# Performance work log

Measured on AMD Instinct MI355X. Metric: run time of the kernel, lower is better.

## Reference

```python
import jax, jax.numpy as jnp
import numpy as np

COMMITMENT_COST = 0.25
N_EMBED = 1024
EMB_DIM = 256

def setup_inputs() -> dict:
    key = jax.random.key(0)
    k1, k2 = jax.random.split(key)
    z = jax.random.normal(k1, (32, EMB_DIM, 32, 32), dtype=jnp.float32)
    # embedding.weight.data.uniform_(-1/n_embed, 1/n_embed)
    embedding = jax.random.uniform(k2, (N_EMBED, EMB_DIM), dtype=jnp.float32,
                                   minval=-1.0 / N_EMBED, maxval=1.0 / N_EMBED)
    return {"z": z, "embedding": embedding}

def reference(z, embedding):
    # NCHW -> NHWC
    zp = jnp.transpose(z, (0, 2, 3, 1))            # [B,H,W,D]
    in_shape = zp.shape
    flat = zp.reshape(-1, in_shape[-1])            # [N,D]
    # squared L2 distances (argmin equivalent to p=2 cdist argmin)
    d2 = (jnp.sum(flat * flat, axis=1, keepdims=True)
          - 2.0 * (flat @ embedding.T)
          + jnp.sum(embedding * embedding, axis=1))  # [N,K]
    idx = jnp.argmin(d2, axis=1)                   # [N]
    # one-hot @ codebook == direct gather
    z_quant = embedding[idx].reshape(in_shape)     # [B,H,W,D]
    codebook_loss = jnp.mean((z_quant - jax.lax.stop_gradient(zp)) ** 2)
    commitment_loss = jnp.mean((zp - jax.lax.stop_gradient(z_quant)) ** 2)
    loss = codebook_loss + COMMITMENT_COST * commitment_loss
    # straight-through estimator
    z_st = zp + jax.lax.stop_gradient(z_quant - zp)
    z_st = jnp.transpose(z_st, (0, 3, 1, 2))       # NHWC -> NCHW
    return (z_st, loss, codebook_loss, commitment_loss)
```

## Files before the change

kernel.cpp:

```cpp
#include <hip/hip_runtime.h>
#include <hip/hip_bf16.h>
#include <stdint.h>


typedef short v8s __attribute__((ext_vector_type(8)));
typedef float v4f __attribute__((ext_vector_type(4)));

__device__ inline unsigned short f2bf(float f) {
    uint32_t u = __float_as_uint(f);
    return (unsigned short)((u + 0x7fffu + ((u >> 16) & 1u)) >> 16);
}

__global__ __launch_bounds__(512) void k_prep_a(const float* __restrict__ z,
                                                unsigned short* __restrict__ Abf) {
    int tid = threadIdx.x;
    int b = blockIdx.x >> 4, hw0 = (blockIdx.x & 15) << 6;
    int t15 = tid & 15, dblk = tid >> 4;
    const float* zp = z + ((size_t)b << 18) + (size_t)(dblk << 3) * 1024 + hw0 + (t15 << 2);
    float4 L[8];
#pragma unroll
    for (int j = 0; j < 8; j++)
        L[j] = *(const float4*)(zp + (size_t)j * 1024);
    const float* Lf = (const float*)L;
    v8s* Aout = (v8s*)Abf + ((size_t)(b * 1024 + hw0 + (t15 << 2))) * 32 + dblk;
#pragma unroll
    for (int c = 0; c < 4; c++) {
        union { v8s v; unsigned short s[8]; } u;
#pragma unroll
        for (int j = 0; j < 8; j++) u.s[j] = f2bf(Lf[j * 4 + c]);
        Aout[(size_t)c * 32] = u.v;
    }
}

__global__ __launch_bounds__(256) void k_prep_e(const float* __restrict__ E,
                                                unsigned short* __restrict__ Ebf,
                                                float* __restrict__ nE,
                                                float* __restrict__ accum) {
    int k = blockIdx.x, tid = threadIdx.x;
    float v = E[(size_t)k * 256 + tid];
    Ebf[(size_t)k * 256 + tid] = f2bf(v);
    float s = v * v;
#pragma unroll
    for (int off = 1; off < 64; off <<= 1) s += __shfl_xor(s, off);
    __shared__ float w4[4];
    if ((tid & 63) == 0) w4[tid >> 6] = s;
    __syncthreads();
    if (tid == 0) {
        nE[k] = 0.5f * (w4[0] + w4[1] + w4[2] + w4[3]);
        if (k == 0) accum[0] = 0.f;
    }
}

__global__ __launch_bounds__(512, 4) void k_argmin(
        const unsigned short* __restrict__ Abf,
        const unsigned short* __restrict__ Ebf,
        const float* __restrict__ nE,
        unsigned long long* __restrict__ cand) {
    __shared__ v8s B[4096];
    int tid = threadIdx.x;
    int lane = tid & 63, w = tid >> 6;
    int g = lane >> 4, m = lane & 15;
    int split = blockIdx.x & 7;
    int R0 = (blockIdx.x >> 3) << 8;
    int C0 = split << 7;

    const v8s* Ep = (const v8s*)Ebf;
#pragma unroll
    for (int k = 0; k < 8; k++) {
        int u = tid + (k << 9);
        int um = u & 15, ug = (u >> 4) & 3, udc = (u >> 6) & 7, uct = u >> 9;
        B[u] = Ep[(size_t)(C0 + uct * 16 + um) * 32 + udc * 4 + ug];
    }
    float ne[8];
#pragma unroll
    for (int ct = 0; ct < 8; ct++) ne[ct] = nE[C0 + ct * 16 + m];

    v8s a[2][8];
    const v8s* Ap = (const v8s*)Abf;
    int rbase = R0 + w * 32;
#pragma unroll
    for (int s = 0; s < 2; s++) {
        int row = rbase + s * 16 + m;
#pragma unroll
        for (int dc = 0; dc < 8; dc++)
            a[s][dc] = Ap[(size_t)row * 32 + dc * 4 + g];
    }
    __syncthreads();

    float best[2][4]; int bidx[2][4];
#pragma unroll
    for (int s = 0; s < 2; s++)
#pragma unroll
        for (int r = 0; r < 4; r++) { best[s][r] = 3.4e38f; bidx[s][r] = 0; }

#pragma unroll 1
    for (int ct = 0; ct < 8; ct++) {
        v4f acc0 = {0.f, 0.f, 0.f, 0.f}, acc1 = {0.f, 0.f, 0.f, 0.f};
#pragma unroll
        for (int dc = 0; dc < 8; dc++) {
            v8s bf = B[ct * 512 + dc * 64 + g * 16 + m];
            acc0 = __builtin_amdgcn_mfma_f32_16x16x32_bf16(a[0][dc], bf, acc0, 0, 0, 0);
            acc1 = __builtin_amdgcn_mfma_f32_16x16x32_bf16(a[1][dc], bf, acc1, 0, 0, 0);
        }
        int code = C0 + (ct << 4) + m;
        float nv = ne[ct];
#pragma unroll
        for (int r = 0; r < 4; r++) {
            float s0 = nv - acc0[r];
            if (s0 < best[0][r]) { best[0][r] = s0; bidx[0][r] = code; }
            float s1 = nv - acc1[r];
            if (s1 < best[1][r]) { best[1][r] = s1; bidx[1][r] = code; }
        }
    }

#pragma unroll
    for (int s = 0; s < 2; s++)
#pragma unroll
        for (int r = 0; r < 4; r++) {
            uint32_t sb = __float_as_uint(best[s][r]);
            sb = (sb & 0x80000000u) ? ~sb : (sb | 0x80000000u);
            unsigned long long pk = ((unsigned long long)sb << 32) | (uint32_t)bidx[s][r];
#pragma unroll
            for (int off = 1; off < 16; off <<= 1) {
                unsigned long long o = __shfl_xor(pk, off);
                if (o < pk) pk = o;
            }
            if (m == 0)
                cand[(size_t)split * 32768 + R0 + w * 32 + s * 16 + g * 4 + r] = pk;
        }
}

__global__ __launch_bounds__(256) void k_out(const float* __restrict__ z,
                                             const float* __restrict__ E,
                                             const unsigned long long* __restrict__ cand,
                                             float* __restrict__ out,
                                             float* __restrict__ accum) {
    __shared__ float et[256][33];
    __shared__ int   kk[32];
    __shared__ float w4[4];
    int bid = blockIdx.x;
    int b = bid >> 5, hw0 = (bid & 31) << 5;
    int tid = threadIdx.x;
    if (tid < 32) {
        int n = b * 1024 + hw0 + tid;
        unsigned long long bv = cand[n];
#pragma unroll
        for (int s = 1; s < 8; s++) {
            unsigned long long v = cand[(size_t)s * 32768 + n];
            if (v < bv) bv = v;
        }
        kk[tid] = (int)(bv & 0xffffffffu);
    }
    __syncthreads();
    for (int r = 0; r < 32; r++)
        et[tid][r] = E[(size_t)kk[r] * 256 + tid];
    __syncthreads();

    int c4 = (tid & 7) << 2, dt = tid >> 3;
    const float* zb = z + ((size_t)b << 18);
    float* ob = out + ((size_t)b << 18);
    float lsum = 0.f;
#pragma unroll
    for (int i = 0; i < 8; i++) {
        int d = dt + (i << 5);
        size_t o = (size_t)d * 1024 + hw0 + c4;
        const float4 zv = *(const float4*)(zb + o);
        float4 ev;
        ev.x = et[d][c4]; ev.y = et[d][c4 + 1]; ev.z = et[d][c4 + 2]; ev.w = et[d][c4 + 3];
        *(float4*)(ob + o) = ev;
        float dx = ev.x - zv.x, dy = ev.y - zv.y, dz2 = ev.z - zv.z, dw = ev.w - zv.w;
        lsum += dx * dx + dy * dy + dz2 * dz2 + dw * dw;
    }
#pragma unroll
    for (int off = 1; off < 64; off <<= 1) lsum += __shfl_xor(lsum, off);
    if ((tid & 63) == 0) w4[tid >> 6] = lsum;
    __syncthreads();
    if (tid == 0) atomicAdd(accum, w4[0] + w4[1] + w4[2] + w4[3]);
}

__global__ void k_loss(const float* __restrict__ accum, float* __restrict__ out) {
    if (threadIdx.x == 0) {
        float s = accum[0] * (1.0f / 8388608.0f);
        out[8388608] = 1.25f * s;
        out[8388609] = s;
        out[8388610] = s;
    }
}

extern "C" void kernel_launch(void* const* d_in, const int* in_sizes, int n_in,
                              void* d_out, int out_size, void* d_ws, size_t ws_size,
                              hipStream_t stream) {
    const float* z = (const float*)d_in[0];
    const float* E = (const float*)d_in[1];
    char* ws = (char*)d_ws;
    unsigned short*     Abf   = (unsigned short*)(ws);
    unsigned short*     Ebf   = (unsigned short*)(ws + 16777216);
    float*              nE    = (float*)(ws + 17301504);
    unsigned long long* cand  = (unsigned long long*)(ws + 17305600);
    float*              accum = (float*)(ws + 19402752);
    float* out = (float*)d_out;

    hipLaunchKernelGGL(k_prep_a, dim3(512),  dim3(512), 0, stream, z, Abf);
    hipLaunchKernelGGL(k_prep_e, dim3(1024), dim3(256), 0, stream, E, Ebf, nE, accum);
    hipLaunchKernelGGL(k_argmin, dim3(1024), dim3(512), 0, stream, Abf, Ebf, nE, cand);
    hipLaunchKernelGGL(k_out,    dim3(1024), dim3(256), 0, stream, z, E, cand, out, accum);
    hipLaunchKernelGGL(k_loss,   dim3(1),    dim3(64),  0, stream, accum, out);
}
```

Measured before the change: 141.1 us.

## Fuse argmin and output gather into one kernel with double-buffered codebook staging

Merges the distance/argmin kernel and the gather/loss kernel into one. Each block now owns 64 rows across all 1024 codes, so the 8-way code split, the candidate buffer and the cross-split reduction are gone. Codebook tiles are streamed into LDS through double-buffered global_load_lds while the MFMAs run. The cost is that every block rereads the whole bf16 codebook, and the grid drops to 512 blocks of 256 threads, which may leave the GPU less occupied.

```diff
diff --git a/kernel.cpp b/kernel.cpp
--- a/kernel.cpp
+++ b/kernel.cpp
@@ -51,131 +51,138 @@
     }
 }
 
-__global__ __launch_bounds__(512, 4) void k_argmin(
+__global__ __launch_bounds__(256, 2) void k_main(
         const unsigned short* __restrict__ Abf,
         const unsigned short* __restrict__ Ebf,
         const float* __restrict__ nE,
-        unsigned long long* __restrict__ cand) {
-    __shared__ v8s B[4096];
+        const float* __restrict__ z,
+        const float* __restrict__ E,
+        float* __restrict__ out,
+        float* __restrict__ accum) {
+    __shared__ union {
+        v8s   B[2][2048];
+        float Eg[32][260];
+    } S;
+    __shared__ int   idxLds[64];
+    __shared__ float w4[4];
+
     int tid = threadIdx.x;
     int lane = tid & 63, w = tid >> 6;
     int g = lane >> 4, m = lane & 15;
-    int split = blockIdx.x & 7;
-    int R0 = (blockIdx.x >> 3) << 8;
-    int C0 = split << 7;
+    int R0 = blockIdx.x << 6;
+    int b = R0 >> 10, hw0 = R0 & 1023;
+
+    v8s a[8];
+    {
+        const v8s* Ap = (const v8s*)Abf;
+        int row = R0 + w * 16 + m;
+#pragma unroll
+        for (int dc = 0; dc < 8; dc++)
+            a[dc] = Ap[(size_t)row * 32 + dc * 4 + g];
+    }
 
     const v8s* Ep = (const v8s*)Ebf;
-#pragma unroll
-    for (int k = 0; k < 8; k++) {
-        int u = tid + (k << 9);
-        int um = u & 15, ug = (u >> 4) & 3, udc = (u >> 6) & 7, uct = u >> 9;
-        B[u] = Ep[(size_t)(C0 + uct * 16 + um) * 32 + udc * 4 + ug];
-    }
-    float ne[8];
-#pragma unroll
-    for (int ct = 0; ct < 8; ct++) ne[ct] = nE[C0 + ct * 16 + m];
-
-    v8s a[2][8];
-    const v8s* Ap = (const v8s*)Abf;
-    int rbase = R0 + w * 32;
-#pragma unroll
-    for (int s = 0; s < 2; s++) {
-        int row = rbase + s * 16 + m;
-#pragma unroll
-        for (int dc = 0; dc < 8; dc++)
-            a[s][dc] = Ap[(size_t)row * 32 + dc * 4 + g];
+#define STAGE(ch, bufSel)                                                     \
+    {                                                                         \
+        _Pragma("unroll")                                                     \
+        for (int k = 0; k < 8; k++) {                                         \
+            int u  = (((w << 3) + k) << 6) + lane;                            \
+            int um = u & 15, ug = (u >> 4) & 3;                               \
+            int udc = (u >> 6) & 7, uct = (u >> 9) & 3;                       \
+            const v8s* gp = Ep + ((size_t)((ch) * 64 + uct * 16 + um) * 32    \
+                                  + udc * 4 + ug);                            \
+            __builtin_amdgcn_global_load_lds(                                 \
+                (const __attribute__((address_space(1))) void*)gp,            \
+                (__attribute__((address_space(3))) void*)                     \
+                    &S.B[bufSel][((w << 3) + k) << 6],                        \
+                16, 0, 0);                                                    \
+        }                                                                     \
+    }
+
+    float best[4]; int bidx[4];
+#pragma unroll
+    for (int r = 0; r < 4; r++) { best[r] = 3.4e38f; bidx[r] = 0; }
+
+    STAGE(0, 0);
+#pragma unroll 1
+    for (int ct = 0; ct < 16; ct++) {
+        int cur = ct & 1;
+        __syncthreads();
+        if (ct < 15) STAGE(ct + 1, cur ^ 1);
+        float ne4[4];
+#pragma unroll
+        for (int t = 0; t < 4; t++) ne4[t] = nE[ct * 64 + t * 16 + m];
+#pragma unroll
+        for (int t = 0; t < 4; t++) {
+            v4f acc = {0.f, 0.f, 0.f, 0.f};
+#pragma unroll
+            for (int dc = 0; dc < 8; dc++) {
+                v8s bf = S.B[cur][t * 512 + dc * 64 + g * 16 + m];
+                acc = __builtin_amdgcn_mfma_f32_16x16x32_bf16(a[dc], bf, acc, 0, 0, 0);
+            }
+            int code = ct * 64 + t * 16 + m;
+#pragma unroll
+            for (int r = 0; r < 4; r++) {
+                float s = ne4[t] - acc[r];
+                if (s < best[r]) { best[r] = s; bidx[r] = code; }
+            }
+        }
+    }
+
+#pragma unroll
+    for (int r = 0; r < 4; r++) {
+        uint32_t sb = __float_as_uint(best[r]);
+        sb = (sb & 0x80000000u) ? ~sb : (sb | 0x80000000u);
+        unsigned long long pk = ((unsigned long long)sb << 32) | (uint32_t)bidx[r];
+#pragma unroll
+        for (int off = 1; off < 16; off <<= 1) {
+            unsigned long long o = __shfl_xor(pk, off);
+            if (o < pk) pk = o;
+        }
+        if (m == 0)
+            idxLds[w * 16 + g * 4 + r] = (int)(pk & 0xffffffffu);
     }
     __syncthreads();
 
-    float best[2][4]; int bidx[2][4];
-#pragma unroll
-    for (int s = 0; s < 2; s++)
-#pragma unroll
-        for (int r = 0; r < 4; r++) { best[s][r] = 3.4e38f; bidx[s][r] = 0; }
-
-#pragma unroll 1
-    for (int ct = 0; ct < 8; ct++) {
-        v4f acc0 = {0.f, 0.f, 0.f, 0.f}, acc1 = {0.f, 0.f, 0.f, 0.f};
-#pragma unroll
-        for (int dc = 0; dc < 8; dc++) {
-            v8s bf = B[ct * 512 + dc * 64 + g * 16 + m];
-            acc0 = __builtin_amdgcn_mfma_f32_16x16x32_bf16(a[0][dc], bf, acc0, 0, 0, 0);
-            acc1 = __builtin_amdgcn_mfma_f32_16x16x32_bf16(a[1][dc], bf, acc1, 0, 0, 0);
-        }
-        int code = C0 + (ct << 4) + m;
-        float nv = ne[ct];
-#pragma unroll
-        for (int r = 0; r < 4; r++) {
-            float s0 = nv - acc0[r];
-            if (s0 < best[0][r]) { best[0][r] = s0; bidx[0][r] = code; }
-            float s1 = nv - acc1[r];
-            if (s1 < best[1][r]) { best[1][r] = s1; bidx[1][r] = code; }
-        }
-    }
-
-#pragma unroll
-    for (int s = 0; s < 2; s++)
-#pragma unroll
-        for (int r = 0; r < 4; r++) {
-            uint32_t sb = __float_as_uint(best[s][r]);
-            sb = (sb & 0x80000000u) ? ~sb : (sb | 0x80000000u);
-            unsigned long long pk = ((unsigned long long)sb << 32) | (uint32_t)bidx[s][r];
-#pragma unroll
-            for (int off = 1; off < 16; off <<= 1) {
-                unsigned long long o = __shfl_xor(pk, off);
-                if (o < pk) pk = o;
-            }
-            if (m == 0)
-                cand[(size_t)split * 32768 + R0 + w * 32 + s * 16 + g * 4 + r] = pk;
-        }
-}
-
-__global__ __launch_bounds__(256) void k_out(const float* __restrict__ z,
-                                             const float* __restrict__ E,
-                                             const unsigned long long* __restrict__ cand,
-                                             float* __restrict__ out,
-                                             float* __restrict__ accum) {
-    __shared__ float et[256][33];
-    __shared__ int   kk[32];
-    __shared__ float w4[4];
-    int bid = blockIdx.x;
-    int b = bid >> 5, hw0 = (bid & 31) << 5;
-    int tid = threadIdx.x;
-    if (tid < 32) {
-        int n = b * 1024 + hw0 + tid;
-        unsigned long long bv = cand[n];
-#pragma unroll
-        for (int s = 1; s < 8; s++) {
-            unsigned long long v = cand[(size_t)s * 32768 + n];
-            if (v < bv) bv = v;
-        }
-        kk[tid] = (int)(bv & 0xffffffffu);
-    }
-    __syncthreads();
-    for (int r = 0; r < 32; r++)
-        et[tid][r] = E[(size_t)kk[r] * 256 + tid];
-    __syncthreads();
-
-    int c4 = (tid & 7) << 2, dt = tid >> 3;
+    float lsum = 0.f;
     const float* zb = z + ((size_t)b << 18);
     float* ob = out + ((size_t)b << 18);
-    float lsum = 0.f;
-#pragma unroll
-    for (int i = 0; i < 8; i++) {
-        int d = dt + (i << 5);
-        size_t o = (size_t)d * 1024 + hw0 + c4;
-        const float4 zv = *(const float4*)(zb + o);
-        float4 ev;
-        ev.x = et[d][c4]; ev.y = et[d][c4 + 1]; ev.z = et[d][c4 + 2]; ev.w = et[d][c4 + 3];
-        *(float4*)(ob + o) = ev;
-        float dx = ev.x - zv.x, dy = ev.y - zv.y, dz2 = ev.z - zv.z, dw = ev.w - zv.w;
-        lsum += dx * dx + dy * dy + dz2 * dz2 + dw * dw;
+#pragma unroll 1
+    for (int h = 0; h < 2; h++) {
+        {
+            int j2 = tid >> 3, dq = tid & 7;
+            int k = idxLds[h * 32 + j2];
+            const float* ep = E + (size_t)k * 256 + (dq << 2);
+#pragma unroll
+            for (int i = 0; i < 8; i++)
+                *(float4*)&S.Eg[j2][(dq << 2) + i * 32] =
+                    *(const float4*)(ep + i * 32);
+        }
+        __syncthreads();
+        {
+            int jj = (tid & 7) << 2, dt = tid >> 3;
+#pragma unroll
+            for (int i = 0; i < 8; i++) {
+                int d = dt + (i << 5);
+                size_t o = (size_t)d * 1024 + hw0 + (h << 5) + jj;
+                float4 zv = *(const float4*)(zb + o);
+                float4 ev;
+                ev.x = S.Eg[jj + 0][d]; ev.y = S.Eg[jj + 1][d];
+                ev.z = S.Eg[jj + 2][d]; ev.w = S.Eg[jj + 3][d];
+                *(float4*)(ob + o) = ev;
+                float dx = ev.x - zv.x, dy = ev.y - zv.y;
+                float dz2 = ev.z - zv.z, dw = ev.w - zv.w;
+                lsum += dx * dx + dy * dy + dz2 * dz2 + dw * dw;
+            }
+        }
+        __syncthreads();
     }
 #pragma unroll
     for (int off = 1; off < 64; off <<= 1) lsum += __shfl_xor(lsum, off);
     if ((tid & 63) == 0) w4[tid >> 6] = lsum;
     __syncthreads();
     if (tid == 0) atomicAdd(accum, w4[0] + w4[1] + w4[2] + w4[3]);
+#undef STAGE
 }
 
 __global__ void k_loss(const float* __restrict__ accum, float* __restrict__ out) {
@@ -193,16 +200,15 @@
     const float* z = (const float*)d_in[0];
     const float* E = (const float*)d_in[1];
     char* ws = (char*)d_ws;
-    unsigned short*     Abf   = (unsigned short*)(ws);
-    unsigned short*     Ebf   = (unsigned short*)(ws + 16777216);
-    float*              nE    = (float*)(ws + 17301504);
-    unsigned long long* cand  = (unsigned long long*)(ws + 17305600);
-    float*              accum = (float*)(ws + 19402752);
+    unsigned short* Abf   = (unsigned short*)(ws);
+    unsigned short* Ebf   = (unsigned short*)(ws + 16777216);
+    float*          nE    = (float*)(ws + 17301504);
+    float*          accum = (float*)(ws + 17305600);
     float* out = (float*)d_out;
 
+    hipLaunchKernelGGL(k_prep_e, dim3(1024), dim3(256), 0, stream, E, Ebf, nE, accum);
     hipLaunchKernelGGL(k_prep_a, dim3(512),  dim3(512), 0, stream, z, Abf);
-    hipLaunchKernelGGL(k_prep_e, dim3(1024), dim3(256), 0, stream, E, Ebf, nE, accum);
-    hipLaunchKernelGGL(k_argmin, dim3(1024), dim3(512), 0, stream, Abf, Ebf, nE, cand);
-    hipLaunchKernelGGL(k_out,    dim3(1024), dim3(256), 0, stream, z, E, cand, out, accum);
+    hipLaunchKernelGGL(k_main,   dim3(512),  dim3(256), 0, stream,
+                       Abf, Ebf, nE, z, E, out, accum);
     hipLaunchKernelGGL(k_loss,   dim3(1),    dim3(64),  0, stream, accum, out);
 }
```

Result: no change. 141.0 us (-0.1%).
